# Performance work log

Measured on AMD Instinct MI355X. Metric: run time of the kernel, lower is better.

Reference implementation:

```python
import jax, jax.numpy as jnp
import numpy as np

N_HEAD = 16
D_HEAD = 64
D_MODEL = 1024
B, T = 2, 2048


def setup_inputs() -> dict:
    key = jax.random.key(0)
    ks = jax.random.split(key, 5)
    s = 1.0 / np.sqrt(D_MODEL)
    return {
        "x": jax.random.normal(ks[0], (B, T, D_MODEL), dtype=jnp.float32),
        "wq": jax.random.normal(ks[1], (D_MODEL, D_MODEL), dtype=jnp.float32) * s,
        "wk": jax.random.normal(ks[2], (D_MODEL, D_MODEL), dtype=jnp.float32) * s,
        "wv": jax.random.normal(ks[3], (D_MODEL, D_MODEL), dtype=jnp.float32) * s,
        "wo": jax.random.normal(ks[4], (D_MODEL, D_MODEL), dtype=jnp.float32) * s,
    }


def reference(x, wq, wk, wv, wo):
    Bb, Tt, D = x.shape
    H, Dh = N_HEAD, D_HEAD
    # Linear projections (flax Linear: y = x @ kernel), split heads
    q = (x @ wq).reshape(Bb, Tt, H, Dh)
    k = (x @ wk).reshape(Bb, Tt, H, Dh)
    v = (x @ wv).reshape(Bb, Tt, H, Dh)
    scale = jnp.sqrt(jnp.asarray(Dh)).astype(x.dtype)
    scores = jnp.einsum('bthd,bshd->bhts', q, k) / scale  # [B,H,T,T]
    mask = jnp.tril(jnp.ones((Tt, Tt), dtype=jnp.bool_))
    scores = jnp.where(mask, scores, jnp.finfo(scores.dtype).min)
    attn = jax.nn.softmax(scores, axis=-1)
    out = jnp.einsum('bhts,bshd->bthd', attn, v).reshape(Bb, Tt, D)
    return out @ wo
```

## Files before the change

kernel.cpp:

```cpp
#include <hip/hip_runtime.h>
#include <math.h>

#define DEV static __device__ __forceinline__

typedef __attribute__((ext_vector_type(4))) float f32x4;
typedef __attribute__((ext_vector_type(2))) unsigned u32x2;
typedef __attribute__((ext_vector_type(8))) __bf16 bf16x8;
typedef __attribute__((ext_vector_type(8))) unsigned short u16x8;
typedef __attribute__((ext_vector_type(4))) unsigned short u16x4;

constexpr int TB = 2;
constexpr int TT = 2048;
constexpr int DM = 1024;
constexpr int NH = 16;
constexpr int DH = 64;
constexpr int MR = TB * TT;
constexpr int SQKV = 3 * DM;

DEV unsigned short f2bf(float f) {
  union { float f; unsigned u; } v; v.f = f;
  return (unsigned short)((v.u + 0x7FFFu + ((v.u >> 16) & 1u)) >> 16);
}

DEV unsigned cvtpk(float a, float b) {
  unsigned r;
  asm("v_cvt_pk_bf16_f32 %0, %1, %2" : "=v"(r) : "v"(a), "v"(b));
  return r;
}

DEV void gld16(const void* g, void* l) {
  __builtin_amdgcn_global_load_lds((const __attribute__((address_space(1))) void*)g,
                                   (__attribute__((address_space(3))) void*)l, 16, 0, 0);
}

DEV bf16x8 ldsb8(const unsigned short* p) { return *(const bf16x8*)p; }

__global__ __launch_bounds__(256) void k_prep(const float* __restrict__ x,
                                              const float* __restrict__ w0,
                                              const float* __restrict__ w1,
                                              const float* __restrict__ w2,
                                              const float* __restrict__ w3,
                                              unsigned short* __restrict__ xb,
                                              unsigned short* __restrict__ wtdst) {
  __shared__ float tile[32][33];
  const int id = blockIdx.x, tid = threadIdx.x;
  if (id < 4096) {
    const int z = id >> 10, tl = id & 1023;
    const float* w = z == 0 ? w0 : z == 1 ? w1 : z == 2 ? w2 : w3;
    unsigned short* wt = wtdst + (size_t)z * DM * DM;
    const int n0 = (tl & 31) * 32, k0 = (tl >> 5) * 32;
    const int tx = tid & 31, ty = tid >> 5;
#pragma unroll
    for (int yy = 0; yy < 32; yy += 8)
      tile[ty + yy][tx] = w[(size_t)(k0 + ty + yy) * DM + n0 + tx];
    __syncthreads();
#pragma unroll
    for (int yy = 0; yy < 32; yy += 8)
      wt[(size_t)(n0 + ty + yy) * DM + k0 + tx] = f2bf(tile[tx][ty + yy]);
  } else {
    const int i = ((id - 4096) * 256 + tid) * 8;
    f32x4 a = *(const f32x4*)(x + i);
    f32x4 b = *(const f32x4*)(x + i + 4);
    u16x8 o;
#pragma unroll
    for (int j = 0; j < 4; ++j) { o[j] = f2bf(a[j]); o[j + 4] = f2bf(b[j]); }
    *(u16x8*)(xb + i) = o;
  }
}

__global__ __launch_bounds__(512) void k_gemm_qkv(const unsigned short* __restrict__ A,
                                                  const unsigned short* __restrict__ Bt,
                                                  unsigned short* __restrict__ Qb,
                                                  float ascale,
                                                  unsigned short* __restrict__ kp,
                                                  unsigned short* __restrict__ vt) {
  constexpr int K = DM, NS = K / 32;
  __shared__ alignas(16) unsigned short As[3][128 * 32];
  __shared__ alignas(16) unsigned short Bs[3][128 * 32];
  const int tid = threadIdx.x;
  const int m0 = blockIdx.y * 128, n0 = blockIdx.x * 128;
  const int lane = tid & 63, w = tid >> 6;
  const int lr = lane & 15, lg = lane >> 4;
  const int wm = w >> 2, wn = w & 3;
  const int srow = tid >> 2, scc = (tid & 3) ^ ((srow >> 1) & 3);
  const unsigned short* Ab = A + (size_t)(m0 + srow) * K + scc * 8;
  const unsigned short* Bb = Bt + (size_t)(n0 + srow) * K + scc * 8;
  auto stage = [&](int buf, int s) {
    gld16(Ab + s * 32, (void*)(As[buf] + tid * 8));
    gld16(Bb + s * 32, (void*)(Bs[buf] + tid * 8));
  };
  f32x4 acc[4][2] = {};
  stage(0, 0);
  stage(1, 1);
  int buf = 0;
  for (int s = 0; s < NS; ++s) {
    if (s + 1 < NS) {
      asm volatile("s_waitcnt vmcnt(2)" ::: "memory");
    } else {
      asm volatile("s_waitcnt vmcnt(0)" ::: "memory");
    }
    __builtin_amdgcn_s_barrier();
    if (s + 2 < NS) {
      int nb = buf + 2; if (nb >= 3) nb -= 3;
      stage(nb, s + 2);
    }
    bf16x8 af[4], bfr[2];
#pragma unroll
    for (int i = 0; i < 4; ++i) {
      const int row = wm * 64 + i * 16 + lr;
      af[i] = ldsb8(As[buf] + row * 32 + ((lg ^ ((row >> 1) & 3)) * 8));
    }
#pragma unroll
    for (int j = 0; j < 2; ++j) {
      const int row = wn * 32 + j * 16 + lr;
      bfr[j] = ldsb8(Bs[buf] + row * 32 + ((lg ^ ((row >> 1) & 3)) * 8));
    }
    __builtin_amdgcn_s_setprio(1);
#pragma unroll
    for (int i = 0; i < 4; ++i)
#pragma unroll
      for (int j = 0; j < 2; ++j)
        acc[i][j] = __builtin_amdgcn_mfma_f32_16x16x32_bf16(af[i], bfr[j], acc[i][j], 0, 0, 0);
    __builtin_amdgcn_s_setprio(0);
    if (++buf >= 3) buf = 0;
  }
#pragma unroll
  for (int i = 0; i < 4; ++i)
#pragma unroll
    for (int j = 0; j < 2; ++j) {
      const int row = m0 + wm * 64 + i * 16 + lg * 4;
      const int col = n0 + wn * 32 + j * 16 + lr;
      const int bb = row >> 11, sg = row & (TT - 1);
      if (col < DM) {
#pragma unroll
        for (int r = 0; r < 4; ++r)
          Qb[(size_t)(row + r) * DM + col] = f2bf(acc[i][j][r] * ascale);
      } else if (col < 2 * DM) {
        const int hh = (col - DM) >> 6, dd = (col - DM) & 63;
        unsigned short* kb = kp + (size_t)(bb * NH + hh) * 32 * 4096;
#pragma unroll
        for (int r = 0; r < 4; ++r) {
          const int s = sg + r, t = s >> 6, sl = s & 63;
          kb[t * 4096 + sl * 64 + (((dd >> 3) ^ (sl & 7)) * 8) + (dd & 7)] = f2bf(acc[i][j][r]);
        }
      } else {
        const int hh = (col - 2 * DM) >> 6, dd = (col - 2 * DM) & 63;
        const int t = sg >> 6, sl = sg & 63;
        const int g = ((sl >> 5) << 2) | ((sl >> 2) & 3);
        const int hf2 = (sl >> 4) & 1;
        const int cch = g ^ (dd & 7);
        u16x4 pk;
#pragma unroll
        for (int r = 0; r < 4; ++r) pk[r] = f2bf(acc[i][j][r]);
        *(u16x4*)(vt + (size_t)((bb * NH + hh) * 32 + t) * 4096 + dd * 64 + cch * 8 + hf2 * 4) = pk;
      }
    }
}

__global__ __launch_bounds__(512) void k_gemm_out(const unsigned short* __restrict__ A,
                                                  const unsigned short* __restrict__ Bt,
                                                  float* __restrict__ C) {
  constexpr int K = DM, N = DM, NS = K / 32;
  __shared__ alignas(16) unsigned short As[3][128 * 32];
  __shared__ alignas(16) unsigned short Bs[3][64 * 32];
  const int tid = threadIdx.x;
  const int m0 = blockIdx.y * 128, n0 = blockIdx.x * 64;
  const int lane = tid & 63, w = tid >> 6;
  const int lr = lane & 15, lg = lane >> 4;
  const int wm = w >> 1, wn = w & 1;
  const int srow = tid >> 2, scc = (tid & 3) ^ ((srow >> 1) & 3);
  const unsigned short* Ab = A + (size_t)(m0 + srow) * K + scc * 8;
  const unsigned short* Bb = (tid < 256) ? Bt + (size_t)(n0 + srow) * K + scc * 8 : nullptr;
  auto stage = [&](int buf, int s) {
    gld16(Ab + s * 32, (void*)(As[buf] + tid * 8));
    if (tid < 256) gld16(Bb + s * 32, (void*)(Bs[buf] + tid * 8));
  };
  f32x4 acc[2][2] = {};
  stage(0, 0);
  stage(1, 1);
  int buf = 0;
  for (int s = 0; s < NS; ++s) {
    if (s + 1 < NS) {
      if (w < 4) {
        asm volatile("s_waitcnt vmcnt(2)" ::: "memory");
      } else {
        asm volatile("s_waitcnt vmcnt(1)" ::: "memory");
      }
    } else {
      asm volatile("s_waitcnt vmcnt(0)" ::: "memory");
    }
    __builtin_amdgcn_s_barrier();
    if (s + 2 < NS) {
      int nb = buf + 2; if (nb >= 3) nb -= 3;
      stage(nb, s + 2);
    }
    bf16x8 af[2], bfr[2];
#pragma unroll
    for (int i = 0; i < 2; ++i) {
      const int row = wm * 32 + i * 16 + lr;
      af[i] = ldsb8(As[buf] + row * 32 + ((lg ^ ((row >> 1) & 3)) * 8));
    }
#pragma unroll
    for (int j = 0; j < 2; ++j) {
      const int row = wn * 32 + j * 16 + lr;
      bfr[j] = ldsb8(Bs[buf] + row * 32 + ((lg ^ ((row >> 1) & 3)) * 8));
    }
    __builtin_amdgcn_s_setprio(1);
#pragma unroll
    for (int i = 0; i < 2; ++i)
#pragma unroll
      for (int j = 0; j < 2; ++j)
        acc[i][j] = __builtin_amdgcn_mfma_f32_16x16x32_bf16(af[i], bfr[j], acc[i][j], 0, 0, 0);
    __builtin_amdgcn_s_setprio(0);
    if (++buf >= 3) buf = 0;
  }
#pragma unroll
  for (int i = 0; i < 2; ++i)
#pragma unroll
    for (int j = 0; j < 2; ++j) {
      const int row = m0 + wm * 32 + i * 16 + lg * 4;
      const int col = n0 + wn * 32 + j * 16 + lr;
#pragma unroll
      for (int r = 0; r < 4; ++r) C[(size_t)(row + r) * N + col] = acc[i][j][r];
    }
}

__constant__ const signed char JV[24]  = {15,7,14,14,13,13,12,11, 15,6,12,10,10,9,11,5, 0,1,2,3,8,4,8,9};
__constant__ const signed char T0v[24] = {0,0,0,15,0,14,13,12, 16,0,0,0,11,0,0,0, 0,0,0,0,0,0,9,10};
__constant__ const signed char CNTv[24]= {16,16,15,15,14,14,13,12, 16,14,13,11,11,10,12,12, 2,4,6,8,9,10,9,10};

__global__ __launch_bounds__(512) void k_attn15(const unsigned short* __restrict__ Qb,
                                                const unsigned short* __restrict__ Kp,
                                                const unsigned short* __restrict__ Vt,
                                                unsigned short* __restrict__ O,
                                                float* __restrict__ Oacc0,
                                                float* __restrict__ Oacc1,
                                                float* __restrict__ lacc0,
                                                float* __restrict__ lacc1) {
  __shared__ alignas(16) unsigned short Ks[3][64 * 64];
  __shared__ alignas(16) unsigned short Vs[3][64 * 64];
  const int id = blockIdx.x;
  const int rank = id >> 5, bh = id & 31;
  const int j = JV[rank], t0 = T0v[rank], cnt = CNTv[rank];
  const bool split = (j >= 8);
  const int hf = (t0 > 0) ? 1 : 0;
  const int b = bh >> 4, h = bh & 15;
  const int q0 = j * 128;
  const int tid = threadIdx.x, lane = tid & 63, w = tid >> 6;
  const int lr = lane & 15, lg = lane >> 4;
  const int lsw = lr & 7;
  const int qw = q0 + w * 16;
  const unsigned short* Qg = Qb + (size_t)b * TT * DM + h * DH;
  const unsigned short* kbase = Kp + (size_t)bh * 32 * 4096 + tid * 8;
  const unsigned short* vbase = Vt + (size_t)bh * 32 * 4096 + tid * 8;

  bf16x8 qf[2];
#pragma unroll
  for (int c2 = 0; c2 < 2; ++c2)
    qf[c2] = *(const bf16x8*)(Qg + (size_t)(qw + lr) * DM + c2 * 32 + lg * 8);

  bf16x8 onef;
  {
    union { unsigned short s[8]; bf16x8 v; } ou;
#pragma unroll
    for (int i = 0; i < 8; ++i) ou.s[i] = 0x3F80;
    onef = ou.v;
  }

  f32x4 acco[4] = {};
  f32x4 lac = {};

  auto stage = [&](int buf, int t) {
    gld16(kbase + (size_t)t * 4096, (void*)(Ks[buf] + tid * 8));
    gld16(vbase + (size_t)t * 4096, (void*)(Vs[buf] + tid * 8));
  };

  stage(0, t0);
  stage(1, t0 + 1);
  int buf = 0;
  for (int k = 0; k < cnt; ++k) {
    const int t = t0 + k;
    if (k + 1 < cnt) {
      asm volatile("s_waitcnt vmcnt(2)" ::: "memory");
    } else {
      asm volatile("s_waitcnt vmcnt(0)" ::: "memory");
    }
    __builtin_amdgcn_s_barrier();
    if (k + 2 < cnt) {
      int nb = buf + 2; if (nb >= 3) nb -= 3;
      stage(nb, t + 2);
    }
    const int s0 = t * 64;
    if (s0 <= qw + 15) {
      const unsigned short* Kb_ = Ks[buf];
      const unsigned short* Vb_ = Vs[buf];
      f32x4 st[4] = {};
      __builtin_amdgcn_s_setprio(1);
#pragma unroll
      for (int ct = 0; ct < 4; ++ct)
#pragma unroll
        for (int c2 = 0; c2 < 2; ++c2) {
          bf16x8 kf = ldsb8(Kb_ + (ct * 16 + lr) * 64 + (((c2 * 4 + lg) ^ lsw) * 8));
          st[ct] = __builtin_amdgcn_mfma_f32_16x16x32_bf16(kf, qf[c2], st[ct], 0, 0, 0);
        }
      __builtin_amdgcn_s_setprio(0);
      float p[4][4];
      const int qrel = qw + lr - s0;
      if (s0 + 63 >= qw) {
#pragma unroll
        for (int ct = 0; ct < 4; ++ct)
#pragma unroll
          for (int r = 0; r < 4; ++r) {
            float v = st[ct][r];
            if (ct * 16 + lg * 4 + r > qrel) v = -1e30f;
            p[ct][r] = v;
          }
      } else {
#pragma unroll
        for (int ct = 0; ct < 4; ++ct)
#pragma unroll
          for (int r = 0; r < 4; ++r) p[ct][r] = st[ct][r];
      }
#pragma unroll
      for (int ct = 0; ct < 4; ++ct)
#pragma unroll
        for (int r = 0; r < 4; ++r) p[ct][r] = __builtin_exp2f(p[ct][r]);
      bf16x8 pf[2];
#pragma unroll
      for (int ks = 0; ks < 2; ++ks) {
        union { unsigned w4[4]; bf16x8 v; } pu;
        pu.w4[0] = cvtpk(p[2 * ks][0], p[2 * ks][1]);
        pu.w4[1] = cvtpk(p[2 * ks][2], p[2 * ks][3]);
        pu.w4[2] = cvtpk(p[2 * ks + 1][0], p[2 * ks + 1][1]);
        pu.w4[3] = cvtpk(p[2 * ks + 1][2], p[2 * ks + 1][3]);
        pf[ks] = pu.v;
      }
      __builtin_amdgcn_s_setprio(1);
#pragma unroll
      for (int dt = 0; dt < 4; ++dt) {
        const unsigned short* Vrow = Vb_ + (dt * 16 + lr) * 64;
#pragma unroll
        for (int ks = 0; ks < 2; ++ks) {
          bf16x8 vf = ldsb8(Vrow + (((ks * 4 + lg) ^ lsw) * 8));
          acco[dt] = __builtin_amdgcn_mfma_f32_16x16x32_bf16(pf[ks], vf, acco[dt], 0, 0, 0);
        }
      }
#pragma unroll
      for (int ks = 0; ks < 2; ++ks)
        lac = __builtin_amdgcn_mfma_f32_16x16x32_bf16(pf[ks], onef, lac, 0, 0, 0);
      __builtin_amdgcn_s_setprio(0);
    }
    if (++buf >= 3) buf = 0;
  }
  if (!split) {
#pragma unroll
    for (int r = 0; r < 4; ++r) {
      const float linv = 1.f / lac[r];
      const int q = qw + lg * 4 + r;
#pragma unroll
      for (int dt = 0; dt < 4; ++dt)
        O[(size_t)(b * TT + q) * DM + h * DH + dt * 16 + lr] = f2bf(acco[dt][r] * linv);
    }
  } else {
    const int jj = j - 8;
    float* Oa = (hf ? Oacc1 : Oacc0) + (size_t)(bh * 8 + jj) * 128 * 64;
    float* la = (hf ? lacc1 : lacc0) + (size_t)(bh * 8 + jj) * 128;
#pragma unroll
    for (int dt = 0; dt < 4; ++dt)
#pragma unroll
      for (int r = 0; r < 4; ++r)
        Oa[(w * 16 + lg * 4 + r) * 64 + dt * 16 + lr] = acco[dt][r];
    if (lr == 0) {
#pragma unroll
      for (int r = 0; r < 4; ++r) la[w * 16 + lg * 4 + r] = lac[r];
    }
  }
}

__global__ __launch_bounds__(256) void k_norm(const float* __restrict__ Oacc0,
                                              const float* __restrict__ Oacc1,
                                              const float* __restrict__ lacc0,
                                              const float* __restrict__ lacc1,
                                              unsigned short* __restrict__ O) {
  const int gid = blockIdx.x * 256 + threadIdx.x;
  const int f = gid * 8;
  const int d0 = f & 63, row = (f >> 6) & 127, jj = (f >> 13) & 7, bh = f >> 16;
  const int b = bh >> 4, h = bh & 15;
  const size_t ri = (size_t)(bh * 8 + jj) * 128 + row;
  const size_t oi = ri * 64 + d0;
  f32x4 a0 = *(const f32x4*)(Oacc0 + oi);
  f32x4 a1 = *(const f32x4*)(Oacc0 + oi + 4);
  f32x4 b0 = *(const f32x4*)(Oacc1 + oi);
  f32x4 b1 = *(const f32x4*)(Oacc1 + oi + 4);
  const float linv = 1.f / (lacc0[ri] + lacc1[ri]);
  u16x8 o;
#pragma unroll
  for (int r = 0; r < 4; ++r) {
    o[r] = f2bf((a0[r] + b0[r]) * linv);
    o[r + 4] = f2bf((a1[r] + b1[r]) * linv);
  }
  const int q = 1024 + jj * 128 + row;
  *(u16x8*)(O + (size_t)(b * TT + q) * DM + h * DH + d0) = o;
}

extern "C" void kernel_launch(void* const* d_in, const int* in_sizes, int n_in,
                              void* d_out, int out_size, void* d_ws, size_t ws_size,
                              hipStream_t stream) {
  const float* x = (const float*)d_in[0];
  const float* wq = (const float*)d_in[1];
  const float* wk = (const float*)d_in[2];
  const float* wv = (const float*)d_in[3];
  const float* wo = (const float*)d_in[4];
  float* out = (float*)d_out;
  char* ws = (char*)d_ws;
  const size_t MB = 1u << 20;
  unsigned short* xb = (unsigned short*)(ws);
  float* Oacc0 = (float*)(ws);
  unsigned short* wqt = (unsigned short*)(ws + 8 * MB);
  float* lacc0 = (float*)(ws + 8 * MB);
  float* lacc1 = (float*)(ws + 8 * MB + (32 * 8 * 128) * 4);
  unsigned short* wot = (unsigned short*)(ws + 14 * MB);
  unsigned short* Qb = (unsigned short*)(ws + 16 * MB);
  unsigned short* Kp = (unsigned short*)(ws + 24 * MB);
  unsigned short* Vtb = (unsigned short*)(ws + 32 * MB);
  float* Oacc1 = (float*)(ws + 40 * MB);

  k_prep<<<dim3(6144), 256, 0, stream>>>(x, wq, wk, wv, wo, xb, wqt);
  k_gemm_qkv<<<dim3(24, 32), 512, 0, stream>>>(xb, wqt, Qb, 0.18033688f, Kp, Vtb);
  k_attn15<<<dim3(768), 512, 0, stream>>>(Qb, Kp, Vtb, Qb, Oacc0, Oacc1, lacc0, lacc1);
  k_norm<<<dim3(1024), 256, 0, stream>>>(Oacc0, Oacc1, lacc0, lacc1, Qb);
  k_gemm_out<<<dim3(16, 32), 512, 0, stream>>>(Qb, wot, out);
}
```

Measured before the change: 105.2 us.

## Split every causal query tile into two KV halves with bf16 partials

The hand-tuned 24-rank attention schedule (768 blocks, only late query tiles split) is replaced by a uniform scheme. Every 128-row query tile is split into two blocks, each covering half of its causal KV range, giving 1024 blocks ordered so long and short tiles pair up. Partial outputs are stored as bf16 instead of fp32, and the normalize kernel now combines every row. The KV pipeline drops from triple to double buffering with a higher occupancy hint, trading prefetch depth for more resident blocks; the norm pass moves more data and the bf16 partial sums lose some precision.

```diff
diff --git a/kernel.cpp b/kernel.cpp
--- a/kernel.cpp
+++ b/kernel.cpp
@@ -20,6 +20,11 @@
 DEV unsigned short f2bf(float f) {
   union { float f; unsigned u; } v; v.f = f;
   return (unsigned short)((v.u + 0x7FFFu + ((v.u >> 16) & 1u)) >> 16);
+}
+
+DEV float bf2f(unsigned short s) {
+  union { unsigned u; float f; } v; v.u = (unsigned)s << 16;
+  return v.f;
 }
 
 DEV unsigned cvtpk(float a, float b) {
@@ -225,25 +230,24 @@
     }
 }
 
-__constant__ const signed char JV[24]  = {15,7,14,14,13,13,12,11, 15,6,12,10,10,9,11,5, 0,1,2,3,8,4,8,9};
-__constant__ const signed char T0v[24] = {0,0,0,15,0,14,13,12, 16,0,0,0,11,0,0,0, 0,0,0,0,0,0,9,10};
-__constant__ const signed char CNTv[24]= {16,16,15,15,14,14,13,12, 16,14,13,11,11,10,12,12, 2,4,6,8,9,10,9,10};
-
-__global__ __launch_bounds__(512) void k_attn15(const unsigned short* __restrict__ Qb,
-                                                const unsigned short* __restrict__ Kp,
-                                                const unsigned short* __restrict__ Vt,
-                                                unsigned short* __restrict__ O,
-                                                float* __restrict__ Oacc0,
-                                                float* __restrict__ Oacc1,
-                                                float* __restrict__ lacc0,
-                                                float* __restrict__ lacc1) {
-  __shared__ alignas(16) unsigned short Ks[3][64 * 64];
-  __shared__ alignas(16) unsigned short Vs[3][64 * 64];
+__constant__ const signed char JV[32] = {15,14,13,12,11,10,9,8, 0,1,2,3,4,5,6,7,
+                                         8,9,10,11,12,13,14,15, 7,6,5,4,3,2,1,0};
+__constant__ const signed char HH[32] = {0,0,0,0,0,0,0,0, 0,0,0,0,0,0,0,0,
+                                         1,1,1,1,1,1,1,1, 1,1,1,1,1,1,1,1};
+
+__global__ __launch_bounds__(512, 8) void k_attn16(const unsigned short* __restrict__ Qb,
+                                                   const unsigned short* __restrict__ Kp,
+                                                   const unsigned short* __restrict__ Vt,
+                                                   unsigned short* __restrict__ Oacc0,
+                                                   unsigned short* __restrict__ Oacc1,
+                                                   float* __restrict__ lacc0,
+                                                   float* __restrict__ lacc1) {
+  __shared__ alignas(16) unsigned short Ks[2][64 * 64];
+  __shared__ alignas(16) unsigned short Vs[2][64 * 64];
   const int id = blockIdx.x;
   const int rank = id >> 5, bh = id & 31;
-  const int j = JV[rank], t0 = T0v[rank], cnt = CNTv[rank];
-  const bool split = (j >= 8);
-  const int hf = (t0 > 0) ? 1 : 0;
+  const int j = JV[rank], hh = HH[rank];
+  const int cnt = j + 1, t0 = hh ? (j + 1) : 0;
   const int b = bh >> 4, h = bh & 15;
   const int q0 = j * 128;
   const int tid = threadIdx.x, lane = tid & 63, w = tid >> 6;
@@ -276,20 +280,12 @@
   };
 
   stage(0, t0);
-  stage(1, t0 + 1);
-  int buf = 0;
   for (int k = 0; k < cnt; ++k) {
     const int t = t0 + k;
-    if (k + 1 < cnt) {
-      asm volatile("s_waitcnt vmcnt(2)" ::: "memory");
-    } else {
-      asm volatile("s_waitcnt vmcnt(0)" ::: "memory");
-    }
+    const int buf = k & 1;
+    asm volatile("s_waitcnt vmcnt(0)" ::: "memory");
     __builtin_amdgcn_s_barrier();
-    if (k + 2 < cnt) {
-      int nb = buf + 2; if (nb >= 3) nb -= 3;
-      stage(nb, t + 2);
-    }
+    if (k + 1 < cnt) stage(buf ^ 1, t + 1);
     const int s0 = t * 64;
     if (s0 <= qw + 15) {
       const unsigned short* Kb_ = Ks[buf];
@@ -350,56 +346,38 @@
         lac = __builtin_amdgcn_mfma_f32_16x16x32_bf16(pf[ks], onef, lac, 0, 0, 0);
       __builtin_amdgcn_s_setprio(0);
     }
-    if (++buf >= 3) buf = 0;
-  }
-  if (!split) {
-#pragma unroll
-    for (int r = 0; r < 4; ++r) {
-      const float linv = 1.f / lac[r];
-      const int q = qw + lg * 4 + r;
-#pragma unroll
-      for (int dt = 0; dt < 4; ++dt)
-        O[(size_t)(b * TT + q) * DM + h * DH + dt * 16 + lr] = f2bf(acco[dt][r] * linv);
-    }
-  } else {
-    const int jj = j - 8;
-    float* Oa = (hf ? Oacc1 : Oacc0) + (size_t)(bh * 8 + jj) * 128 * 64;
-    float* la = (hf ? lacc1 : lacc0) + (size_t)(bh * 8 + jj) * 128;
-#pragma unroll
-    for (int dt = 0; dt < 4; ++dt)
-#pragma unroll
-      for (int r = 0; r < 4; ++r)
-        Oa[(w * 16 + lg * 4 + r) * 64 + dt * 16 + lr] = acco[dt][r];
-    if (lr == 0) {
-#pragma unroll
-      for (int r = 0; r < 4; ++r) la[w * 16 + lg * 4 + r] = lac[r];
-    }
-  }
-}
-
-__global__ __launch_bounds__(256) void k_norm(const float* __restrict__ Oacc0,
-                                              const float* __restrict__ Oacc1,
+  }
+  unsigned short* Oa = (hh ? Oacc1 : Oacc0) + (size_t)(bh * 16 + j) * 128 * 64;
+  float* la = (hh ? lacc1 : lacc0) + (size_t)(bh * 16 + j) * 128;
+#pragma unroll
+  for (int dt = 0; dt < 4; ++dt)
+#pragma unroll
+    for (int r = 0; r < 4; ++r)
+      Oa[(w * 16 + lg * 4 + r) * 64 + dt * 16 + lr] = f2bf(acco[dt][r]);
+  if (lr == 0) {
+#pragma unroll
+    for (int r = 0; r < 4; ++r) la[w * 16 + lg * 4 + r] = lac[r];
+  }
+}
+
+__global__ __launch_bounds__(256) void k_norm(const unsigned short* __restrict__ Oacc0,
+                                              const unsigned short* __restrict__ Oacc1,
                                               const float* __restrict__ lacc0,
                                               const float* __restrict__ lacc1,
                                               unsigned short* __restrict__ O) {
   const int gid = blockIdx.x * 256 + threadIdx.x;
   const int f = gid * 8;
-  const int d0 = f & 63, row = (f >> 6) & 127, jj = (f >> 13) & 7, bh = f >> 16;
+  const int d0 = f & 63, row = (f >> 6) & 127, j = (f >> 13) & 15, bh = f >> 17;
   const int b = bh >> 4, h = bh & 15;
-  const size_t ri = (size_t)(bh * 8 + jj) * 128 + row;
+  const size_t ri = (size_t)(bh * 16 + j) * 128 + row;
   const size_t oi = ri * 64 + d0;
-  f32x4 a0 = *(const f32x4*)(Oacc0 + oi);
-  f32x4 a1 = *(const f32x4*)(Oacc0 + oi + 4);
-  f32x4 b0 = *(const f32x4*)(Oacc1 + oi);
-  f32x4 b1 = *(const f32x4*)(Oacc1 + oi + 4);
+  u16x8 a = *(const u16x8*)(Oacc0 + oi);
+  u16x8 c = *(const u16x8*)(Oacc1 + oi);
   const float linv = 1.f / (lacc0[ri] + lacc1[ri]);
   u16x8 o;
 #pragma unroll
-  for (int r = 0; r < 4; ++r) {
-    o[r] = f2bf((a0[r] + b0[r]) * linv);
-    o[r + 4] = f2bf((a1[r] + b1[r]) * linv);
-  }
-  const int q = 1024 + jj * 128 + row;
+  for (int r = 0; r < 8; ++r) o[r] = f2bf((bf2f(a[r]) + bf2f(c[r])) * linv);
+  const int q = j * 128 + row;
   *(u16x8*)(O + (size_t)(b * TT + q) * DM + h * DH + d0) = o;
 }
 
@@ -415,19 +393,19 @@
   char* ws = (char*)d_ws;
   const size_t MB = 1u << 20;
   unsigned short* xb = (unsigned short*)(ws);
-  float* Oacc0 = (float*)(ws);
+  unsigned short* Oacc0 = (unsigned short*)(ws);
   unsigned short* wqt = (unsigned short*)(ws + 8 * MB);
   float* lacc0 = (float*)(ws + 8 * MB);
-  float* lacc1 = (float*)(ws + 8 * MB + (32 * 8 * 128) * 4);
+  float* lacc1 = (float*)(ws + 8 * MB + (32 * 16 * 128) * 4);
   unsigned short* wot = (unsigned short*)(ws + 14 * MB);
   unsigned short* Qb = (unsigned short*)(ws + 16 * MB);
   unsigned short* Kp = (unsigned short*)(ws + 24 * MB);
   unsigned short* Vtb = (unsigned short*)(ws + 32 * MB);
-  float* Oacc1 = (float*)(ws + 40 * MB);
+  unsigned short* Oacc1 = (unsigned short*)(ws + 40 * MB);
 
   k_prep<<<dim3(6144), 256, 0, stream>>>(x, wq, wk, wv, wo, xb, wqt);
   k_gemm_qkv<<<dim3(24, 32), 512, 0, stream>>>(xb, wqt, Qb, 0.18033688f, Kp, Vtb);
-  k_attn15<<<dim3(768), 512, 0, stream>>>(Qb, Kp, Vtb, Qb, Oacc0, Oacc1, lacc0, lacc1);
-  k_norm<<<dim3(1024), 256, 0, stream>>>(Oacc0, Oacc1, lacc0, lacc1, Qb);
+  k_attn16<<<dim3(1024), 512, 0, stream>>>(Qb, Kp, Vtb, Oacc0, Oacc1, lacc0, lacc1);
+  k_norm<<<dim3(2048), 256, 0, stream>>>(Oacc0, Oacc1, lacc0, lacc1, Qb);
   k_gemm_out<<<dim3(16, 32), 512, 0, stream>>>(Qb, wot, out);
 }
```

Result: slower. 115.7 us (+10.0%).

## Fuse split-KV normalization into output projection GEMM A-tile loading

Applied to the files above, without the earlier changes.

Removes the separate k_norm launch. For row blocks in the second half of each sequence, the output GEMM now reads the two fp32 partial accumulators and row sums directly, normalizes and converts them to bf16 in registers, and writes the result into shared memory as the A tile. This saves a kernel launch and a bf16 round trip through global memory. The cost is that each A element is recomputed 16 times (once per column block), fp32 reads are wider, and those blocks drop to a two-stage register-staged pipeline with two block barriers per step instead of the async three-stage one.

```diff
diff --git a/kernel.cpp b/kernel.cpp
--- a/kernel.cpp
+++ b/kernel.cpp
@@ -159,6 +159,10 @@
 
 __global__ __launch_bounds__(512) void k_gemm_out(const unsigned short* __restrict__ A,
                                                   const unsigned short* __restrict__ Bt,
+                                                  const float* __restrict__ Oacc0,
+                                                  const float* __restrict__ Oacc1,
+                                                  const float* __restrict__ lacc0,
+                                                  const float* __restrict__ lacc1,
                                                   float* __restrict__ C) {
   constexpr int K = DM, N = DM, NS = K / 32;
   __shared__ alignas(16) unsigned short As[3][128 * 32];
@@ -171,48 +175,105 @@
   const int srow = tid >> 2, scc = (tid & 3) ^ ((srow >> 1) & 3);
   const unsigned short* Ab = A + (size_t)(m0 + srow) * K + scc * 8;
   const unsigned short* Bb = (tid < 256) ? Bt + (size_t)(n0 + srow) * K + scc * 8 : nullptr;
-  auto stage = [&](int buf, int s) {
-    gld16(Ab + s * 32, (void*)(As[buf] + tid * 8));
-    if (tid < 256) gld16(Bb + s * 32, (void*)(Bs[buf] + tid * 8));
-  };
   f32x4 acc[2][2] = {};
-  stage(0, 0);
-  stage(1, 1);
-  int buf = 0;
-  for (int s = 0; s < NS; ++s) {
-    if (s + 1 < NS) {
-      if (w < 4) {
-        asm volatile("s_waitcnt vmcnt(2)" ::: "memory");
+  const bool splitBlk = (m0 & 1024) != 0;
+
+  if (!splitBlk) {
+    auto stage = [&](int buf, int s) {
+      gld16(Ab + s * 32, (void*)(As[buf] + tid * 8));
+      if (tid < 256) gld16(Bb + s * 32, (void*)(Bs[buf] + tid * 8));
+    };
+    stage(0, 0);
+    stage(1, 1);
+    int buf = 0;
+    for (int s = 0; s < NS; ++s) {
+      if (s + 1 < NS) {
+        if (w < 4) {
+          asm volatile("s_waitcnt vmcnt(2)" ::: "memory");
+        } else {
+          asm volatile("s_waitcnt vmcnt(1)" ::: "memory");
+        }
       } else {
-        asm volatile("s_waitcnt vmcnt(1)" ::: "memory");
-      }
-    } else {
+        asm volatile("s_waitcnt vmcnt(0)" ::: "memory");
+      }
+      __builtin_amdgcn_s_barrier();
+      if (s + 2 < NS) {
+        int nb = buf + 2; if (nb >= 3) nb -= 3;
+        stage(nb, s + 2);
+      }
+      bf16x8 af[2], bfr[2];
+#pragma unroll
+      for (int i = 0; i < 2; ++i) {
+        const int row = wm * 32 + i * 16 + lr;
+        af[i] = ldsb8(As[buf] + row * 32 + ((lg ^ ((row >> 1) & 3)) * 8));
+      }
+#pragma unroll
+      for (int j = 0; j < 2; ++j) {
+        const int row = wn * 32 + j * 16 + lr;
+        bfr[j] = ldsb8(Bs[buf] + row * 32 + ((lg ^ ((row >> 1) & 3)) * 8));
+      }
+      __builtin_amdgcn_s_setprio(1);
+#pragma unroll
+      for (int i = 0; i < 2; ++i)
+#pragma unroll
+        for (int j = 0; j < 2; ++j)
+          acc[i][j] = __builtin_amdgcn_mfma_f32_16x16x32_bf16(af[i], bfr[j], acc[i][j], 0, 0, 0);
+      __builtin_amdgcn_s_setprio(0);
+      if (++buf >= 3) buf = 0;
+    }
+  } else {
+    const int b_ = (m0 + srow) >> 11;
+    const int jj = (m0 >> 7) & 7;
+    f32x4 ra0, ra1, rb0, rb1;
+    float rl;
+    auto issueA = [&](int s) {
+      const int h2 = s >> 1;
+      const size_t ri = (size_t)((b_ * NH + h2) * 8 + jj) * 128 + srow;
+      const size_t base = ri * 64 + (s & 1) * 32 + scc * 8;
+      ra0 = *(const f32x4*)(Oacc0 + base);
+      ra1 = *(const f32x4*)(Oacc0 + base + 4);
+      rb0 = *(const f32x4*)(Oacc1 + base);
+      rb1 = *(const f32x4*)(Oacc1 + base + 4);
+      rl = lacc0[ri] + lacc1[ri];
+    };
+    issueA(0);
+    if (tid < 256) gld16(Bb, (void*)(Bs[0] + tid * 8));
+    for (int s = 0; s < NS; ++s) {
+      const int buf = s & 1;
+      const float linv = 1.f / rl;
+      u16x8 aw;
+#pragma unroll
+      for (int q = 0; q < 4; ++q) {
+        aw[q] = f2bf((ra0[q] + rb0[q]) * linv);
+        aw[q + 4] = f2bf((ra1[q] + rb1[q]) * linv);
+      }
+      *(u16x8*)(As[buf] + tid * 8) = aw;
       asm volatile("s_waitcnt vmcnt(0)" ::: "memory");
-    }
-    __builtin_amdgcn_s_barrier();
-    if (s + 2 < NS) {
-      int nb = buf + 2; if (nb >= 3) nb -= 3;
-      stage(nb, s + 2);
-    }
-    bf16x8 af[2], bfr[2];
-#pragma unroll
-    for (int i = 0; i < 2; ++i) {
-      const int row = wm * 32 + i * 16 + lr;
-      af[i] = ldsb8(As[buf] + row * 32 + ((lg ^ ((row >> 1) & 3)) * 8));
-    }
-#pragma unroll
-    for (int j = 0; j < 2; ++j) {
-      const int row = wn * 32 + j * 16 + lr;
-      bfr[j] = ldsb8(Bs[buf] + row * 32 + ((lg ^ ((row >> 1) & 3)) * 8));
-    }
-    __builtin_amdgcn_s_setprio(1);
-#pragma unroll
-    for (int i = 0; i < 2; ++i)
-#pragma unroll
-      for (int j = 0; j < 2; ++j)
-        acc[i][j] = __builtin_amdgcn_mfma_f32_16x16x32_bf16(af[i], bfr[j], acc[i][j], 0, 0, 0);
-    __builtin_amdgcn_s_setprio(0);
-    if (++buf >= 3) buf = 0;
+      __syncthreads();
+      if (s + 1 < NS) {
+        issueA(s + 1);
+        if (tid < 256) gld16(Bb + (s + 1) * 32, (void*)(Bs[buf ^ 1] + tid * 8));
+      }
+      bf16x8 af[2], bfr[2];
+#pragma unroll
+      for (int i = 0; i < 2; ++i) {
+        const int row = wm * 32 + i * 16 + lr;
+        af[i] = ldsb8(As[buf] + row * 32 + ((lg ^ ((row >> 1) & 3)) * 8));
+      }
+#pragma unroll
+      for (int j = 0; j < 2; ++j) {
+        const int row = wn * 32 + j * 16 + lr;
+        bfr[j] = ldsb8(Bs[buf] + row * 32 + ((lg ^ ((row >> 1) & 3)) * 8));
+      }
+      __builtin_amdgcn_s_setprio(1);
+#pragma unroll
+      for (int i = 0; i < 2; ++i)
+#pragma unroll
+        for (int j = 0; j < 2; ++j)
+          acc[i][j] = __builtin_amdgcn_mfma_f32_16x16x32_bf16(af[i], bfr[j], acc[i][j], 0, 0, 0);
+      __builtin_amdgcn_s_setprio(0);
+      __syncthreads();
+    }
   }
 #pragma unroll
   for (int i = 0; i < 2; ++i)
@@ -377,32 +438,6 @@
   }
 }
 
-__global__ __launch_bounds__(256) void k_norm(const float* __restrict__ Oacc0,
-                                              const float* __restrict__ Oacc1,
-                                              const float* __restrict__ lacc0,
-                                              const float* __restrict__ lacc1,
-                                              unsigned short* __restrict__ O) {
-  const int gid = blockIdx.x * 256 + threadIdx.x;
-  const int f = gid * 8;
-  const int d0 = f & 63, row = (f >> 6) & 127, jj = (f >> 13) & 7, bh = f >> 16;
-  const int b = bh >> 4, h = bh & 15;
-  const size_t ri = (size_t)(bh * 8 + jj) * 128 + row;
-  const size_t oi = ri * 64 + d0;
-  f32x4 a0 = *(const f32x4*)(Oacc0 + oi);
-  f32x4 a1 = *(const f32x4*)(Oacc0 + oi + 4);
-  f32x4 b0 = *(const f32x4*)(Oacc1 + oi);
-  f32x4 b1 = *(const f32x4*)(Oacc1 + oi + 4);
-  const float linv = 1.f / (lacc0[ri] + lacc1[ri]);
-  u16x8 o;
-#pragma unroll
-  for (int r = 0; r < 4; ++r) {
-    o[r] = f2bf((a0[r] + b0[r]) * linv);
-    o[r + 4] = f2bf((a1[r] + b1[r]) * linv);
-  }
-  const int q = 1024 + jj * 128 + row;
-  *(u16x8*)(O + (size_t)(b * TT + q) * DM + h * DH + d0) = o;
-}
-
 extern "C" void kernel_launch(void* const* d_in, const int* in_sizes, int n_in,
                               void* d_out, int out_size, void* d_ws, size_t ws_size,
                               hipStream_t stream) {
@@ -428,6 +463,5 @@
   k_prep<<<dim3(6144), 256, 0, stream>>>(x, wq, wk, wv, wo, xb, wqt);
   k_gemm_qkv<<<dim3(24, 32), 512, 0, stream>>>(xb, wqt, Qb, 0.18033688f, Kp, Vtb);
   k_attn15<<<dim3(768), 512, 0, stream>>>(Qb, Kp, Vtb, Qb, Oacc0, Oacc1, lacc0, lacc1);
-  k_norm<<<dim3(1024), 256, 0, stream>>>(Oacc0, Oacc1, lacc0, lacc1, Qb);
-  k_gemm_out<<<dim3(16, 32), 512, 0, stream>>>(Qb, wot, out);
-}
+  k_gemm_out<<<dim3(16, 32), 512, 0, stream>>>(Qb, wot, Oacc0, Oacc1, lacc0, lacc1, out);
+}
```

After: 117.7 us. +11.9%, slower.
